# Optimization experiments

Hardware: AMD Instinct MI355X
Metric: run time of the kernel (lower is better)

The kernel has to match this reference:

```python
import jax, jax.numpy as jnp
import numpy as np

B, T, V, E, H, NC = 256, 512, 128, 128, 256, 10000


def setup_inputs() -> dict:
    key = jax.random.key(0)
    ks = jax.random.split(key, 10)
    return {
        "dec_input_batch": jax.random.randint(ks[0], (B, T), 0, V),
        "dec_input_lengths": jax.random.randint(ks[1], (B,), 1, T + 1),
        "max_prob_clusters": jax.random.randint(ks[2], (B,), 0, NC),
        "char_embeddings": jax.random.normal(ks[3], (V, E), dtype=jnp.float32) * 0.1,
        "cluster_embeddings": jax.random.normal(ks[4], (NC, H), dtype=jnp.float32) * 0.1,
        "W0": jax.random.normal(ks[5], (E + H + H, 4 * H), dtype=jnp.float32) * 0.05,
        "b0": jnp.zeros((4 * H,), jnp.float32),
        "W1": jax.random.normal(ks[6], (H + H, 4 * H), dtype=jnp.float32) * 0.05,
        "b1": jnp.zeros((4 * H,), jnp.float32),
        "decoderW": jax.random.normal(ks[7], (H, V), dtype=jnp.float32) * (1.0 / (H + V)),
        "decoderB": jnp.zeros((V,), jnp.float32),
    }


def _lstm_step(c, h, x, W, b):
    # TF BasicLSTMCell: gates order i, j, f, o; forget_bias = 1.0
    z = jnp.concatenate([x, h], axis=-1) @ W + b
    i, j, f, o = jnp.split(z, 4, axis=-1)
    c2 = c * jax.nn.sigmoid(f + 1.0) + jax.nn.sigmoid(i) * jnp.tanh(j)
    h2 = jnp.tanh(c2) * jax.nn.sigmoid(o)
    return c2, h2


def reference(dec_input_batch, dec_input_lengths, max_prob_clusters,
              char_embeddings, cluster_embeddings, W0, b0, W1, b1,
              decoderW, decoderB):
    Bb, Tt = dec_input_batch.shape
    Hh = decoderW.shape[0]
    x = char_embeddings[dec_input_batch]                       # [B,T,E]
    clus = cluster_embeddings[max_prob_clusters]               # [B,H]
    clus_bt = jnp.broadcast_to(clus[:, None, :], (Bb, Tt, clus.shape[-1]))
    x = jnp.concatenate([x, clus_bt], axis=-1)                 # [B,T,E+H]
    xs = jnp.transpose(x, (1, 0, 2))                           # [T,B,E+H]
    # dynamic_rnn sequence_length semantics: past length -> zero output, state copied through
    mask = (jnp.arange(Tt)[:, None] < dec_input_lengths[None, :])[..., None]  # [T,B,1]
    zeros = jnp.zeros((Bb, Hh), x.dtype)

    def step(carry, inp):
        c0, h0, c1, h1 = carry
        xt, m = inp
        c0n, h0n = _lstm_step(c0, h0, xt, W0, b0)
        c1n, h1n = _lstm_step(c1, h1, h0n, W1, b1)
        c0 = jnp.where(m, c0n, c0); h0 = jnp.where(m, h0n, h0)
        c1 = jnp.where(m, c1n, c1); h1 = jnp.where(m, h1n, h1)
        out = jnp.where(m, h1n, jnp.zeros_like(h1n))
        return (c0, h0, c1, h1), out

    _, outs = jax.lax.scan(step, (zeros, zeros, zeros, zeros), (xs, mask))
    outs = jnp.transpose(outs, (1, 0, 2))                      # [B,T,H]
    raw_scores = outs @ decoderW + decoderB                    # [B,T,V]
    return raw_scores
```

## Files before the change

kernel.cpp:

```cpp
#include <hip/hip_runtime.h>

#define B_ 256
#define T_ 512
#define V_ 128
#define E_ 128
#define H_ 256
#define FH 1024

#define GROUPS 32
#define RPG 8
#define CWG 16
#define NWG (GROUPS*CWG)

#define HTG 2048
#define GST (GROUPS*HTG)

typedef float f4 __attribute__((ext_vector_type(4)));

#define OFF_HT0  0
#define OFF_HT1  (OFF_HT0 + 2*GST)
#define OFF_BAR  (OFF_HT1 + 2*GST)
#define BARSZ    (GROUPS*1024)
#define OFF_TP   (OFF_BAR + BARSZ)
#define OFF_CP   (OFF_TP + V_*FH)
#define OFF_WP0  (OFF_CP + B_*FH)
#define OFF_WP1  (OFF_WP0 + CWG*64*64*4)
#define OFF_DWT  (OFF_WP1 + CWG*128*64*4)
#define OFF_B1   (OFF_DWT + V_*H_)

__device__ __forceinline__ int gcol(int c, int col) {
  int u = col >> 2, g = col & 3;
  return g*256 + c*16 + u;
}

__device__ __forceinline__ float sigm(float x){ return 1.f/(1.f+__expf(-x)); }
__device__ __forceinline__ float tanh_(float x){ return 1.f - 2.f/(1.f+__expf(2.f*x)); }


__global__ void prep_pack(const float* __restrict__ W0, const float* __restrict__ W1,
                          const float* __restrict__ dW, const float* __restrict__ b1,
                          float* __restrict__ ws) {
  float* wp0 = ws + OFF_WP0; float* wp1 = ws + OFF_WP1;
  float* dwT = ws + OFF_DWT; float* b1p = ws + OFF_B1;
  const int N0 = CWG*64*64*4;
  const int N1 = CWG*128*64*4;
  const int N2 = V_*H_;
  const int N3 = FH;
  const int total = N0+N1+N2+N3;
  for (int i = blockIdx.x*blockDim.x + threadIdx.x; i < total; i += gridDim.x*blockDim.x) {
    if (i < N0) {
      int cc = i >> 14; int rem = i & 16383;
      int kb = rem >> 8; int ln = (rem >> 2) & 63; int j = i & 3;
      int k = kb*4 + j;
      wp0[i] = W0[(E_+H_+k)*FH + gcol(cc, ln)];
    } else if (i < N0+N1) {
      int idx = i - N0;
      int cc = idx >> 15; int rem = idx & 32767;
      int kb = rem >> 8; int ln = (rem >> 2) & 63; int j = idx & 3;
      int k2 = kb*4 + j;
      wp1[idx] = W1[k2*FH + gcol(cc, ln)];
    } else if (i < N0+N1+N2) {
      int l = i - N0 - N1;
      int v = l >> 8, k = l & 255;
      dwT[l] = dW[k*V_ + v];
    } else {
      int cc2 = i - N0 - N1 - N2;
      b1p[cc2] = b1[gcol(cc2>>6, cc2&63)];
    }
  }
}

__global__ void prep_tok(const float* __restrict__ cemb, const float* __restrict__ W0,
                         float* __restrict__ ws) {
  __shared__ float ce[E_];
  float* TP = ws + OFF_TP;
  int v = blockIdx.x >> 2, q = blockIdx.x & 3;
  int tid = threadIdx.x;
  if (tid < E_) ce[tid] = cemb[v*E_ + tid];
  __syncthreads();
  int ccol = q*256 + tid;
  int G = gcol(ccol>>6, ccol&63);
  float acc = 0.f;
  for (int e = 0; e < E_; ++e) acc = fmaf(ce[e], W0[e*FH + G], acc);
  TP[v*FH + ccol] = acc;
}

__global__ void prep_clus(const int* __restrict__ clus, const float* __restrict__ clemb,
                          const float* __restrict__ W0, const float* __restrict__ b0,
                          float* __restrict__ ws) {
  __shared__ float ce[H_];
  float* CP = ws + OFF_CP;
  int b = blockIdx.x >> 2, q = blockIdx.x & 3;
  int tid = threadIdx.x;
  int cl = clus[b];
  ce[tid] = clemb[(long long)cl*H_ + tid];
  __syncthreads();
  int ccol = q*256 + tid;
  int G = gcol(ccol>>6, ccol&63);
  float acc = b0[G];
  for (int e = 0; e < H_; ++e) acc = fmaf(ce[e], W0[(E_+e)*FH + G], acc);
  CP[b*FH + ccol] = acc;
}


__device__ __forceinline__ void st64(float* p, float a, float b) {
  float2 t; t.x = a; t.y = b;
  __hip_atomic_store((unsigned long long*)p, __builtin_bit_cast(unsigned long long, t),
                     __ATOMIC_RELAXED, __HIP_MEMORY_SCOPE_AGENT);
}

__device__ __forceinline__ unsigned long long ld64(const void* p) {
  return __hip_atomic_load((const unsigned long long*)p, __ATOMIC_RELAXED,
                           __HIP_MEMORY_SCOPE_AGENT);
}

__device__ __forceinline__ void flag_set(unsigned* p, unsigned v) {
  asm volatile("s_waitcnt vmcnt(0)" ::: "memory");
  __hip_atomic_store(p, v, __ATOMIC_RELAXED, __HIP_MEMORY_SCOPE_AGENT);
}

__device__ __forceinline__ void spinAB(const unsigned* fgrp, int lane, unsigned tgt) {
  const unsigned* p = fgrp + (lane & 15)*32 + ((lane >> 5) << 4);
  unsigned v = __hip_atomic_load(p, __ATOMIC_RELAXED, __HIP_MEMORY_SCOPE_AGENT);
  while (!__all((int)(v >= tgt))) {
    __builtin_amdgcn_s_sleep(4);
    v = __hip_atomic_load(p, __ATOMIC_RELAXED, __HIP_MEMORY_SCOPE_AGENT);
  }
}

__device__ __forceinline__ void spinB(const unsigned* fgrp, int lane, unsigned tgt) {
  const unsigned* p = fgrp + (lane & 15)*32 + 16;
  unsigned v = __hip_atomic_load(p, __ATOMIC_RELAXED, __HIP_MEMORY_SCOPE_AGENT);
  while (!__all((int)(v >= tgt))) {
    __builtin_amdgcn_s_sleep(4);
    v = __hip_atomic_load(p, __ATOMIC_RELAXED, __HIP_MEMORY_SCOPE_AGENT);
  }
}

__device__ __forceinline__ void lstm_gate(const f4 z, float& cc, float& hh, const bool upd) {
  float ci = sigm(z.x);
  float cj = tanh_(z.y);
  float cf = sigm(z.z + 1.f);
  float co = sigm(z.w);
  float cn = fmaf(cc, cf, ci*cj);
  float hn = tanh_(cn)*co;
  if (upd) { cc = cn; hh = hn; }
}


__global__ __launch_bounds__(256, 2) void lstm_persist(
    const int* __restrict__ toks, const int* __restrict__ lens,
    const float* __restrict__ decB, float* __restrict__ ws, float* __restrict__ out)
{
  const int blk  = blockIdx.x;
  const int grp  = ((blk & 7) << 2) | (blk >> 7);
  const int c    = (blk >> 3) & 15;
  const int tid  = threadIdx.x;
  const int lane = tid & 63;
  const int wv   = tid >> 6;
  const int cof  = c*64;

  float* ht0 = ws + OFF_HT0;
  float* ht1 = ws + OFF_HT1;
  unsigned* fgrp = (unsigned*)(ws + OFF_BAR) + grp*1024;
  const float* TP   = ws + OFF_TP;
  const float* CP   = ws + OFF_CP;
  const float* wp0c = ws + OFF_WP0 + c*(64*64*4);
  const float* wp1c = ws + OFF_WP1 + c*(128*64*4);
  const float* dwT  = ws + OFF_DWT;
  const float* b1p  = ws + OFF_B1;

  __shared__ __align__(16) float h0s[2048];
  __shared__ __align__(16) float h1s[2048];
  __shared__ __align__(16) float za[4][8][64];
  __shared__ __align__(16) float zb[4][8][64];
  __shared__ float ldsW[8][260];
  __shared__ float pred[4][64];

  for (int i = tid; i < 8*H_; i += 256)
    ldsW[i>>8][i&255] = dwT[(c*8 + (i>>8))*H_ + (i&255)];

  int Lg = lens[grp*RPG + (lane & 7)];
  Lg = max(Lg, __shfl_xor(Lg, 1));
  Lg = max(Lg, __shfl_xor(Lg, 2));
  Lg = max(Lg, __shfl_xor(Lg, 4));

  const int gu = lane & 15, q = lane >> 4;
  const int rowA = grp*RPG + q, rowB = grp*RPG + q + 4;
  const int lenA = lens[rowA], lenB = lens[rowB];
  const int* tokApt = toks + rowA*T_;
  const int* tokBpt = toks + rowB*T_;
  const f4 cpA = *(const f4*)(CP + rowA*FH + cof + gu*4);
  const f4 cpB = *(const f4*)(CP + rowB*FH + cof + gu*4);
  const f4 b1v = *(const f4*)(b1p + cof + gu*4);
  const int puboff = grp*HTG + (c*16 + gu)*8 + q*2;
  float c0A = 0.f, h0A = 0.f, c0B = 0.f, h0B = 0.f;
  float c1A = 0.f, h1A = 0.f, c1B = 0.f, h1B = 0.f;

  const int pm = lane >> 3, pv = lane & 7;
  const int prm = (pm < 4) ? pm*2 : (pm-4)*2 + 1;
  const int plen = lens[grp*RPG + pm];
  const float decb = decB[c*8 + pv];
  float* outp = out + (size_t)(grp*RPG + pm)*T_*V_ + c*8 + pv;

  __syncthreads();

  if (wv == 0) {
    f4 zAv = *(const f4*)(TP + tokApt[0]*FH + cof + gu*4) + cpA;
    f4 zBv = *(const f4*)(TP + tokBpt[0]*FH + cof + gu*4) + cpB;
    lstm_gate(zAv, c0A, h0A, 0 < lenA);
    lstm_gate(zBv, c0B, h0B, 0 < lenB);
    st64(ht0 + puboff, h0A, h0B);
    if (lane == 0) flag_set(fgrp + c*32, 1u);
  } else if (wv == 1) {
    if (lane == 0) flag_set(fgrp + c*32 + 16, 1u);
  }

  for (int t = 0; t < Lg; ++t) {
    const int buf = t & 1;

    f4 tpA = {0,0,0,0}, tpB = {0,0,0,0};
    if (wv == 0 && t + 1 < Lg) {
      tpA = *(const f4*)(TP + tokApt[t+1]*FH + cof + gu*4);
      tpB = *(const f4*)(TP + tokBpt[t+1]*FH + cof + gu*4);
    }

    if (wv == 0) spinAB(fgrp, lane, (unsigned)(t + 1));
    __syncthreads();
    __atomic_signal_fence(__ATOMIC_SEQ_CST);

    {
      const float* s0 = ht0 + buf*GST + grp*HTG + wv*512 + lane*8;
      const float* s1 = ht1 + buf*GST + grp*HTG + wv*512 + lane*8;
      unsigned long long a0 = ld64(s0),   a1 = ld64(s0+2);
      unsigned long long a2 = ld64(s0+4), a3 = ld64(s0+6);
      unsigned long long b0 = ld64(s1),   b1 = ld64(s1+2);
      unsigned long long b2 = ld64(s1+4), b3 = ld64(s1+6);
      float* d0 = h0s + wv*512 + lane*8;
      float* d1 = h1s + wv*512 + lane*8;
      *(unsigned long long*)(d0)   = a0; *(unsigned long long*)(d0+2) = a1;
      *(unsigned long long*)(d0+4) = a2; *(unsigned long long*)(d0+6) = a3;
      *(unsigned long long*)(d1)   = b0; *(unsigned long long*)(d1+2) = b1;
      *(unsigned long long*)(d1+4) = b2; *(unsigned long long*)(d1+6) = b3;
    }

    f4 A0l = {0,0,0,0}, A0h = {0,0,0,0}, A1l = {0,0,0,0}, A1h = {0,0,0,0};
    #pragma unroll 2
    for (int b = 0; b < 16; ++b) {
      const int kb = wv*16 + b;
      const f4 w0 = *(const f4*)(wp0c + kb*256 + lane*4);
      const f4 wl = *(const f4*)(wp1c + kb*256 + lane*4);
      const f4 wu = *(const f4*)(wp1c + (64 + kb)*256 + lane*4);
      #pragma unroll
      for (int j = 0; j < 4; ++j) {
        const int k = kb*4 + j;
        const float* hb0 = h0s + k*8;
        const float* hb1 = h1s + k*8;
        const f4 h0lo = *(const f4*)(hb0);
        const f4 h0hi = *(const f4*)(hb0 + 4);
        const f4 h1lo = *(const f4*)(hb1);
        const f4 h1hi = *(const f4*)(hb1 + 4);
        const float w0j = w0[j], wlj = wl[j], wuj = wu[j];
        A0l += w0j * h0lo;  A0h += w0j * h0hi;
        A1l += wlj * h0lo + wuj * h1lo;
        A1h += wlj * h0hi + wuj * h1hi;
      }
    }

    float pacc = 0.f;
    {
      const int kq = wv*64;
      #pragma unroll 4
      for (int k2 = 0; k2 < 64; k2 += 4) {
        const f4 w4 = *(const f4*)&ldsW[pv][kq + k2];
        pacc = fmaf(h1s[(kq+k2  )*8 + prm], w4.x, pacc);
        pacc = fmaf(h1s[(kq+k2+1)*8 + prm], w4.y, pacc);
        pacc = fmaf(h1s[(kq+k2+2)*8 + prm], w4.z, pacc);
        pacc = fmaf(h1s[(kq+k2+3)*8 + prm], w4.w, pacc);
      }
    }

    #pragma unroll
    for (int r = 0; r < 4; ++r) {
      za[wv][r][lane]     = A0l[r];
      za[wv][4 + r][lane] = A0h[r];
      zb[wv][r][lane]     = A1l[r];
      zb[wv][4 + r][lane] = A1h[r];
    }
    pred[wv][lane] = pacc;
    __syncthreads();

    if (wv == 0) {
      if (t + 1 < Lg) {
        f4 zA = *(const f4*)&za[0][q*2][gu*4];
        zA += *(const f4*)&za[1][q*2][gu*4];
        zA += *(const f4*)&za[2][q*2][gu*4];
        zA += *(const f4*)&za[3][q*2][gu*4];
        f4 zB = *(const f4*)&za[0][q*2+1][gu*4];
        zB += *(const f4*)&za[1][q*2+1][gu*4];
        zB += *(const f4*)&za[2][q*2+1][gu*4];
        zB += *(const f4*)&za[3][q*2+1][gu*4];
        zA += tpA + cpA;
        zB += tpB + cpB;
        lstm_gate(zA, c0A, h0A, (t+1) < lenA);
        lstm_gate(zB, c0B, h0B, (t+1) < lenB);
        st64(ht0 + (buf^1)*GST + puboff, h0A, h0B);
        if (lane == 0) flag_set(fgrp + c*32, (unsigned)(t + 2));
      }
    } else if (wv == 1) {
      f4 zA = *(const f4*)&zb[0][q*2][gu*4];
      zA += *(const f4*)&zb[1][q*2][gu*4];
      zA += *(const f4*)&zb[2][q*2][gu*4];
      zA += *(const f4*)&zb[3][q*2][gu*4];
      f4 zB = *(const f4*)&zb[0][q*2+1][gu*4];
      zB += *(const f4*)&zb[1][q*2+1][gu*4];
      zB += *(const f4*)&zb[2][q*2+1][gu*4];
      zB += *(const f4*)&zb[3][q*2+1][gu*4];
      zA += b1v;
      zB += b1v;
      lstm_gate(zA, c1A, h1A, t < lenA);
      lstm_gate(zB, c1B, h1B, t < lenB);
      st64(ht1 + (buf^1)*GST + puboff, h1A, h1B);
      if (lane == 0) flag_set(fgrp + c*32 + 16, (unsigned)(t + 2));
    } else if (wv == 2) {
      if (t > 0) {
        float tot = pred[0][lane] + pred[1][lane] + pred[2][lane] + pred[3][lane] + decb;
        if (t - 1 < plen) outp[(size_t)(t-1)*V_] = tot;
      }
    }
  }

  if (wv == 0) spinB(fgrp, lane, (unsigned)(Lg + 1));
  __syncthreads();
  __atomic_signal_fence(__ATOMIC_SEQ_CST);
  {
    const float* s1 = ht1 + (size_t)(Lg & 1)*GST + grp*HTG + wv*512 + lane*8;
    unsigned long long b0 = ld64(s1),   b1 = ld64(s1+2);
    unsigned long long b2 = ld64(s1+4), b3 = ld64(s1+6);
    float* d1 = h1s + wv*512 + lane*8;
    *(unsigned long long*)(d1)   = b0; *(unsigned long long*)(d1+2) = b1;
    *(unsigned long long*)(d1+4) = b2; *(unsigned long long*)(d1+6) = b3;
  }
  {
    float pacc = 0.f;
    const int kq = wv*64;
    #pragma unroll 4
    for (int k2 = 0; k2 < 64; k2 += 4) {
      const f4 w4 = *(const f4*)&ldsW[pv][kq + k2];
      pacc = fmaf(h1s[(kq+k2  )*8 + prm], w4.x, pacc);
      pacc = fmaf(h1s[(kq+k2+1)*8 + prm], w4.y, pacc);
      pacc = fmaf(h1s[(kq+k2+2)*8 + prm], w4.z, pacc);
      pacc = fmaf(h1s[(kq+k2+3)*8 + prm], w4.w, pacc);
    }
    pred[wv][lane] = pacc;
  }
  __syncthreads();
  if (wv == 2) {
    float tot = pred[0][lane] + pred[1][lane] + pred[2][lane] + pred[3][lane] + decb;
    if (Lg - 1 < plen) outp[(size_t)(Lg-1)*V_] = tot;
  }
}


extern "C" void kernel_launch(void* const* d_in, const int* in_sizes, int n_in,
                              void* d_out, int out_size, void* d_ws, size_t ws_size,
                              hipStream_t stream) {
  const int*   toks  = (const int*)d_in[0];
  const int*   lens  = (const int*)d_in[1];
  const int*   clus  = (const int*)d_in[2];
  const float* cemb  = (const float*)d_in[3];
  const float* clemb = (const float*)d_in[4];
  const float* W0    = (const float*)d_in[5];
  const float* b0    = (const float*)d_in[6];
  const float* W1    = (const float*)d_in[7];
  const float* b1    = (const float*)d_in[8];
  const float* dW    = (const float*)d_in[9];
  const float* decB  = (const float*)d_in[10];
  float* out = (float*)d_out;
  float* ws  = (float*)d_ws;

  hipMemsetAsync(out, 0, (size_t)B_*T_*V_*sizeof(float), stream);
  hipMemsetAsync(ws, 0, (size_t)(OFF_BAR + BARSZ)*sizeof(float), stream);

  prep_pack<<<1024, 256, 0, stream>>>(W0, W1, dW, b1, ws);
  prep_tok <<<V_*4, 256, 0, stream>>>(cemb, W0, ws);
  prep_clus<<<B_*4, 256, 0, stream>>>(clus, clemb, W0, b0, ws);
  lstm_persist<<<NWG, 256, 0, stream>>>(toks, lens, decB, ws, out);
}
```

Before: 5.421 ms.

## Cache first weight blocks in registers, remap block-to-group mapping, shorten spin sleep

Preloads the first four weight blocks of each wave's recurrent slice into registers once, before the timestep loop, so each step issues fewer global weight loads. Changes the blockIdx-to-(group, column) mapping so the blocks of one group are spread differently within each XCD. Also halves the s_sleep interval in the flag spin-wait loops to react faster to barrier release. The trade-off is higher register pressure, which could hurt occupancy at launch_bounds(256,2), and more polling traffic on the flags.

```diff
diff --git a/kernel.cpp b/kernel.cpp
--- a/kernel.cpp
+++ b/kernel.cpp
@@ -123,7 +123,7 @@
   const unsigned* p = fgrp + (lane & 15)*32 + ((lane >> 5) << 4);
   unsigned v = __hip_atomic_load(p, __ATOMIC_RELAXED, __HIP_MEMORY_SCOPE_AGENT);
   while (!__all((int)(v >= tgt))) {
-    __builtin_amdgcn_s_sleep(4);
+    __builtin_amdgcn_s_sleep(2);
     v = __hip_atomic_load(p, __ATOMIC_RELAXED, __HIP_MEMORY_SCOPE_AGENT);
   }
 }
@@ -132,7 +132,7 @@
   const unsigned* p = fgrp + (lane & 15)*32 + 16;
   unsigned v = __hip_atomic_load(p, __ATOMIC_RELAXED, __HIP_MEMORY_SCOPE_AGENT);
   while (!__all((int)(v >= tgt))) {
-    __builtin_amdgcn_s_sleep(4);
+    __builtin_amdgcn_s_sleep(2);
     v = __hip_atomic_load(p, __ATOMIC_RELAXED, __HIP_MEMORY_SCOPE_AGENT);
   }
 }
@@ -153,8 +153,10 @@
     const float* __restrict__ decB, float* __restrict__ ws, float* __restrict__ out)
 {
   const int blk  = blockIdx.x;
-  const int grp  = ((blk & 7) << 2) | (blk >> 7);
-  const int c    = (blk >> 3) & 15;
+  const int xcd  = blk & 7;
+  const int j    = blk >> 3;
+  const int grp  = (xcd << 2) | ((j + (j >> 4)) & 3);
+  const int c    = (j >> 2) & 15;
   const int tid  = threadIdx.x;
   const int lane = tid & 63;
   const int wv   = tid >> 6;
@@ -202,6 +204,15 @@
   const int plen = lens[grp*RPG + pm];
   const float decb = decB[c*8 + pv];
   float* outp = out + (size_t)(grp*RPG + pm)*T_*V_ + c*8 + pv;
+
+  f4 w0r[4], wlr[4], wur[4];
+  #pragma unroll
+  for (int b = 0; b < 4; ++b) {
+    const int kb = wv*16 + b;
+    w0r[b] = *(const f4*)(wp0c + kb*256 + lane*4);
+    wlr[b] = *(const f4*)(wp1c + kb*256 + lane*4);
+    wur[b] = *(const f4*)(wp1c + (64 + kb)*256 + lane*4);
+  }
 
   __syncthreads();
 
@@ -245,22 +256,40 @@
     }
 
     f4 A0l = {0,0,0,0}, A0h = {0,0,0,0}, A1l = {0,0,0,0}, A1h = {0,0,0,0};
-    #pragma unroll 2
-    for (int b = 0; b < 16; ++b) {
-      const int kb = wv*16 + b;
-      const f4 w0 = *(const f4*)(wp0c + kb*256 + lane*4);
-      const f4 wl = *(const f4*)(wp1c + kb*256 + lane*4);
-      const f4 wu = *(const f4*)(wp1c + (64 + kb)*256 + lane*4);
+
+    #pragma unroll
+    for (int b = 0; b < 4; ++b) {
       #pragma unroll
-      for (int j = 0; j < 4; ++j) {
-        const int k = kb*4 + j;
+      for (int jj = 0; jj < 4; ++jj) {
+        const int k = (wv*16 + b)*4 + jj;
         const float* hb0 = h0s + k*8;
         const float* hb1 = h1s + k*8;
         const f4 h0lo = *(const f4*)(hb0);
         const f4 h0hi = *(const f4*)(hb0 + 4);
         const f4 h1lo = *(const f4*)(hb1);
         const f4 h1hi = *(const f4*)(hb1 + 4);
-        const float w0j = w0[j], wlj = wl[j], wuj = wu[j];
+        const float w0j = w0r[b][jj], wlj = wlr[b][jj], wuj = wur[b][jj];
+        A0l += w0j * h0lo;  A0h += w0j * h0hi;
+        A1l += wlj * h0lo + wuj * h1lo;
+        A1h += wlj * h0hi + wuj * h1hi;
+      }
+    }
+    #pragma unroll 2
+    for (int b = 4; b < 16; ++b) {
+      const int kb = wv*16 + b;
+      const f4 w0 = *(const f4*)(wp0c + kb*256 + lane*4);
+      const f4 wl = *(const f4*)(wp1c + kb*256 + lane*4);
+      const f4 wu = *(const f4*)(wp1c + (64 + kb)*256 + lane*4);
+      #pragma unroll
+      for (int jj = 0; jj < 4; ++jj) {
+        const int k = kb*4 + jj;
+        const float* hb0 = h0s + k*8;
+        const float* hb1 = h1s + k*8;
+        const f4 h0lo = *(const f4*)(hb0);
+        const f4 h0hi = *(const f4*)(hb0 + 4);
+        const f4 h1lo = *(const f4*)(hb1);
+        const f4 h1hi = *(const f4*)(hb1 + 4);
+        const float w0j = w0[jj], wlj = wl[jj], wuj = wu[jj];
         A0l += w0j * h0lo;  A0h += w0j * h0hi;
         A1l += wlj * h0lo + wuj * h1lo;
         A1h += wlj * h0hi + wuj * h1hi;
```

Measured after the change: 9.282 ms. +71.2%, slower.

## Split layer-0 and layer-1 phases to publish h0 before waiting on h1

Applied to the files above, without the earlier changes.

Each step now waits only on layer-0 flags first, computes the layer-0 recurrent matvec, applies the gate and publishes h0 for the next step. Only then does it wait on layer-1 flags and load h1 for the layer-1 matvec. This takes layer 0 off the cross-workgroup critical path so it can run ahead of layer 1, at the cost of an extra __syncthreads per step and reloading h0 from LDS in the second phase. The spin sleep interval is also shortened.

```diff
diff --git a/kernel.cpp b/kernel.cpp
--- a/kernel.cpp
+++ b/kernel.cpp
@@ -119,11 +119,11 @@
   __hip_atomic_store(p, v, __ATOMIC_RELAXED, __HIP_MEMORY_SCOPE_AGENT);
 }
 
-__device__ __forceinline__ void spinAB(const unsigned* fgrp, int lane, unsigned tgt) {
-  const unsigned* p = fgrp + (lane & 15)*32 + ((lane >> 5) << 4);
+__device__ __forceinline__ void spinA(const unsigned* fgrp, int lane, unsigned tgt) {
+  const unsigned* p = fgrp + (lane & 15)*32;
   unsigned v = __hip_atomic_load(p, __ATOMIC_RELAXED, __HIP_MEMORY_SCOPE_AGENT);
   while (!__all((int)(v >= tgt))) {
-    __builtin_amdgcn_s_sleep(4);
+    __builtin_amdgcn_s_sleep(2);
     v = __hip_atomic_load(p, __ATOMIC_RELAXED, __HIP_MEMORY_SCOPE_AGENT);
   }
 }
@@ -132,7 +132,7 @@
   const unsigned* p = fgrp + (lane & 15)*32 + 16;
   unsigned v = __hip_atomic_load(p, __ATOMIC_RELAXED, __HIP_MEMORY_SCOPE_AGENT);
   while (!__all((int)(v >= tgt))) {
-    __builtin_amdgcn_s_sleep(4);
+    __builtin_amdgcn_s_sleep(2);
     v = __hip_atomic_load(p, __ATOMIC_RELAXED, __HIP_MEMORY_SCOPE_AGENT);
   }
 }
@@ -225,45 +225,84 @@
       tpB = *(const f4*)(TP + tokBpt[t+1]*FH + cof + gu*4);
     }
 
-    if (wv == 0) spinAB(fgrp, lane, (unsigned)(t + 1));
+    if (wv == 0) spinA(fgrp, lane, (unsigned)(t + 1));
     __syncthreads();
     __atomic_signal_fence(__ATOMIC_SEQ_CST);
 
     {
       const float* s0 = ht0 + buf*GST + grp*HTG + wv*512 + lane*8;
-      const float* s1 = ht1 + buf*GST + grp*HTG + wv*512 + lane*8;
       unsigned long long a0 = ld64(s0),   a1 = ld64(s0+2);
       unsigned long long a2 = ld64(s0+4), a3 = ld64(s0+6);
+      float* d0 = h0s + wv*512 + lane*8;
+      *(unsigned long long*)(d0)   = a0; *(unsigned long long*)(d0+2) = a1;
+      *(unsigned long long*)(d0+4) = a2; *(unsigned long long*)(d0+6) = a3;
+    }
+
+    f4 A0l = {0,0,0,0}, A0h = {0,0,0,0};
+    #pragma unroll 4
+    for (int b = 0; b < 16; ++b) {
+      const int kb = wv*16 + b;
+      const f4 w0 = *(const f4*)(wp0c + kb*256 + lane*4);
+      #pragma unroll
+      for (int jj = 0; jj < 4; ++jj) {
+        const int k = kb*4 + jj;
+        const f4 h0lo = *(const f4*)(h0s + k*8);
+        const f4 h0hi = *(const f4*)(h0s + k*8 + 4);
+        A0l += w0[jj] * h0lo;
+        A0h += w0[jj] * h0hi;
+      }
+    }
+    #pragma unroll
+    for (int r = 0; r < 4; ++r) {
+      za[wv][r][lane]     = A0l[r];
+      za[wv][4 + r][lane] = A0h[r];
+    }
+
+    if (wv == 1) spinB(fgrp, lane, (unsigned)(t + 1));
+    __syncthreads();
+    __atomic_signal_fence(__ATOMIC_SEQ_CST);
+
+    if (wv == 0 && t + 1 < Lg) {
+      f4 zA = *(const f4*)&za[0][q*2][gu*4];
+      zA += *(const f4*)&za[1][q*2][gu*4];
+      zA += *(const f4*)&za[2][q*2][gu*4];
+      zA += *(const f4*)&za[3][q*2][gu*4];
+      f4 zB = *(const f4*)&za[0][q*2+1][gu*4];
+      zB += *(const f4*)&za[1][q*2+1][gu*4];
+      zB += *(const f4*)&za[2][q*2+1][gu*4];
+      zB += *(const f4*)&za[3][q*2+1][gu*4];
+      zA += tpA + cpA;
+      zB += tpB + cpB;
+      lstm_gate(zA, c0A, h0A, (t+1) < lenA);
+      lstm_gate(zB, c0B, h0B, (t+1) < lenB);
+      st64(ht0 + (buf^1)*GST + puboff, h0A, h0B);
+      if (lane == 0) flag_set(fgrp + c*32, (unsigned)(t + 2));
+    }
+
+    {
+      const float* s1 = ht1 + buf*GST + grp*HTG + wv*512 + lane*8;
       unsigned long long b0 = ld64(s1),   b1 = ld64(s1+2);
       unsigned long long b2 = ld64(s1+4), b3 = ld64(s1+6);
-      float* d0 = h0s + wv*512 + lane*8;
       float* d1 = h1s + wv*512 + lane*8;
-      *(unsigned long long*)(d0)   = a0; *(unsigned long long*)(d0+2) = a1;
-      *(unsigned long long*)(d0+4) = a2; *(unsigned long long*)(d0+6) = a3;
       *(unsigned long long*)(d1)   = b0; *(unsigned long long*)(d1+2) = b1;
       *(unsigned long long*)(d1+4) = b2; *(unsigned long long*)(d1+6) = b3;
     }
 
-    f4 A0l = {0,0,0,0}, A0h = {0,0,0,0}, A1l = {0,0,0,0}, A1h = {0,0,0,0};
+    f4 A1l = {0,0,0,0}, A1h = {0,0,0,0};
     #pragma unroll 2
     for (int b = 0; b < 16; ++b) {
       const int kb = wv*16 + b;
-      const f4 w0 = *(const f4*)(wp0c + kb*256 + lane*4);
       const f4 wl = *(const f4*)(wp1c + kb*256 + lane*4);
       const f4 wu = *(const f4*)(wp1c + (64 + kb)*256 + lane*4);
       #pragma unroll
-      for (int j = 0; j < 4; ++j) {
-        const int k = kb*4 + j;
-        const float* hb0 = h0s + k*8;
-        const float* hb1 = h1s + k*8;
-        const f4 h0lo = *(const f4*)(hb0);
-        const f4 h0hi = *(const f4*)(hb0 + 4);
-        const f4 h1lo = *(const f4*)(hb1);
-        const f4 h1hi = *(const f4*)(hb1 + 4);
-        const float w0j = w0[j], wlj = wl[j], wuj = wu[j];
-        A0l += w0j * h0lo;  A0h += w0j * h0hi;
-        A1l += wlj * h0lo + wuj * h1lo;
-        A1h += wlj * h0hi + wuj * h1hi;
+      for (int jj = 0; jj < 4; ++jj) {
+        const int k = kb*4 + jj;
+        const f4 h0lo = *(const f4*)(h0s + k*8);
+        const f4 h0hi = *(const f4*)(h0s + k*8 + 4);
+        const f4 h1lo = *(const f4*)(h1s + k*8);
+        const f4 h1hi = *(const f4*)(h1s + k*8 + 4);
+        A1l += wl[jj] * h0lo + wu[jj] * h1lo;
+        A1h += wl[jj] * h0hi + wu[jj] * h1hi;
       }
     }
 
@@ -282,32 +321,13 @@
 
     #pragma unroll
     for (int r = 0; r < 4; ++r) {
-      za[wv][r][lane]     = A0l[r];
-      za[wv][4 + r][lane] = A0h[r];
       zb[wv][r][lane]     = A1l[r];
       zb[wv][4 + r][lane] = A1h[r];
     }
     pred[wv][lane] = pacc;
     __syncthreads();
 
-    if (wv == 0) {
-      if (t + 1 < Lg) {
-        f4 zA = *(const f4*)&za[0][q*2][gu*4];
-        zA += *(const f4*)&za[1][q*2][gu*4];
-        zA += *(const f4*)&za[2][q*2][gu*4];
-        zA += *(const f4*)&za[3][q*2][gu*4];
-        f4 zB = *(const f4*)&za[0][q*2+1][gu*4];
-        zB += *(const f4*)&za[1][q*2+1][gu*4];
-        zB += *(const f4*)&za[2][q*2+1][gu*4];
-        zB += *(const f4*)&za[3][q*2+1][gu*4];
-        zA += tpA + cpA;
-        zB += tpB + cpB;
-        lstm_gate(zA, c0A, h0A, (t+1) < lenA);
-        lstm_gate(zB, c0B, h0B, (t+1) < lenB);
-        st64(ht0 + (buf^1)*GST + puboff, h0A, h0B);
-        if (lane == 0) flag_set(fgrp + c*32, (unsigned)(t + 2));
-      }
-    } else if (wv == 1) {
+    if (wv == 1) {
       f4 zA = *(const f4*)&zb[0][q*2][gu*4];
       zA += *(const f4*)&zb[1][q*2][gu*4];
       zA += *(const f4*)&zb[2][q*2][gu*4];
```

After: 6.624 ms. 22.2% more time.
